# Kernel tuning notes

Hardware: AMD Instinct MI355X
Metric: run time of the kernel (lower is better)

Reference implementation:

```python
import jax, jax.numpy as jnp
import numpy as np

N = 50000      # nodes
F = 128        # feature_dim
H = 128        # hidden_dim
E = 1_600_000  # edges
G = 64         # graphs in batch
A = 8          # n_actions


def setup_inputs() -> dict:
    key = jax.random.key(0)
    ks = jax.random.split(key, 12)
    s = 0.05
    return {
        "x": jax.random.normal(ks[0], (N, F), jnp.float32),
        "edge_attr": jax.random.uniform(ks[1], (E, 1), jnp.float32),
        "W_e1": jax.random.normal(ks[2], (3, 1), jnp.float32) * s,
        "b_e1": jnp.zeros((1,), jnp.float32),
        "W_e2": jax.random.normal(ks[3], (1, 1), jnp.float32) * s,
        "b_e2": jnp.zeros((1,), jnp.float32),
        "W_gcn": jax.random.normal(ks[4], (F, H), jnp.float32) * s,
        "b_gcn": jnp.zeros((H,), jnp.float32),
        "W2": jax.random.normal(ks[5], (H, H), jnp.float32) * s,
        "b2": jnp.zeros((H,), jnp.float32),
        "W3": jax.random.normal(ks[6], (H, A), jnp.float32) * s,
        "b3": jnp.zeros((A,), jnp.float32),
        "edge_index": jax.random.randint(ks[7], (2, E), 0, N, jnp.int64),
        "batch": jnp.sort(jax.random.randint(ks[8], (N,), 0, G, jnp.int64)),
    }


def reference(x, edge_attr, W_e1, b_e1, W_e2, b_e2, W_gcn, b_gcn, W2, b2, W3, b3, edge_index, batch):
    # edge MLP: input is [src, dst, edge_attr] per edge -> (E, 3)
    e_feat = jnp.concatenate([edge_index.T.astype(x.dtype), edge_attr], axis=1)
    h = jax.nn.relu(e_feat @ W_e1 + b_e1)
    w = jax.nn.sigmoid(h @ W_e2 + b_e2)[:, 0]  # (E,)

    # GCNConv: add self-loops (weight 1), symmetric normalization
    loop = jnp.arange(N)
    row = jnp.concatenate([edge_index[0], loop])      # source
    col = jnp.concatenate([edge_index[1], loop])      # target
    w_all = jnp.concatenate([w, jnp.ones((N,), w.dtype)])
    deg = jax.ops.segment_sum(w_all, col, num_segments=N)
    safe_deg = jnp.where(deg > 0, deg, 1.0)
    dis = jnp.where(deg > 0, 1.0 / jnp.sqrt(safe_deg), 0.0)  # deg^-1/2, inf->0
    norm = dis[row] * w_all * dis[col]                # (E+N,)

    xw = x @ W_gcn                                    # (N, H)
    msg = norm[:, None] * xw[row]                     # (E+N, H) gather
    conv = jax.ops.segment_sum(msg, col, num_segments=N) + b_gcn  # scatter
    h1 = jax.nn.relu(conv)

    # global_mean_pool over batch index
    sums = jax.ops.segment_sum(h1, batch, num_segments=G)
    cnt = jax.ops.segment_sum(jnp.ones((N,), h1.dtype), batch, num_segments=G)
    pooled = sums / jnp.maximum(cnt, 1.0)[:, None]    # (G, H)

    h2 = jax.nn.relu(pooled @ W2 + b2)
    return h2 @ W3 + b3                               # (G, A)
```

## Files before the change

### kernel.cpp

```cpp
#include <hip/hip_runtime.h>
#include <hip/hip_fp16.h>
#include <math.h>

#define GB 64
#define AD 8
#define NC2 1024
#define BSH 6
#define BS  64
#define NBMAX 1024

typedef _Float16 half8 __attribute__((ext_vector_type(8)));
typedef float    f32x4 __attribute__((ext_vector_type(4)));

__global__ __launch_bounds__(256) void k_hist2(const int* __restrict__ ei,
                                               int* __restrict__ H2,
                                               int E, int ce, int NB) {
    __shared__ int h[NBMAX];
    int c = blockIdx.x;
    for (int b = threadIdx.x; b < NB; b += 256) h[b] = 0;
    __syncthreads();
    int e0 = c * ce, e1 = min(e0 + ce, E);
    int nv = (e1 - e0) & ~3;
    const int4* dst4 = (const int4*)(ei + E + e0);
    for (int v = threadIdx.x; v < (nv >> 2); v += 256) {
        int4 d = dst4[v];
        atomicAdd(&h[d.x >> BSH], 1);
        atomicAdd(&h[d.y >> BSH], 1);
        atomicAdd(&h[d.z >> BSH], 1);
        atomicAdd(&h[d.w >> BSH], 1);
    }
    for (int e = e0 + nv + threadIdx.x; e < e1; e += 256)
        atomicAdd(&h[ei[E + e] >> BSH], 1);
    __syncthreads();
    for (int b = threadIdx.x; b < NB; b += 256)
        H2[(size_t)c * NB + b] = h[b];
}

__global__ __launch_bounds__(256) void k_cscan(int* __restrict__ H2,
                                               int* __restrict__ cntB,
                                               int NB, int nc) {
    __shared__ int ssum[256];
    int b = blockIdx.x;
    int t = threadIdx.x;
    int v[4];
    int local = 0;
    #pragma unroll
    for (int k = 0; k < 4; k++) {
        int c = t * 4 + k;
        v[k] = (c < nc) ? H2[(size_t)c * NB + b] : 0;
        local += v[k];
    }
    ssum[t] = local;
    __syncthreads();
    for (int s = 1; s < 256; s <<= 1) {
        int tmp = (t >= s) ? ssum[t - s] : 0;
        __syncthreads();
        ssum[t] += tmp;
        __syncthreads();
    }
    int run = ssum[t] - local;
    #pragma unroll
    for (int k = 0; k < 4; k++) {
        int c = t * 4 + k;
        if (c < nc) H2[(size_t)c * NB + b] = run;
        run += v[k];
    }
    if (t == 255) cntB[b] = ssum[255];
}

__global__ __launch_bounds__(1024) void k_bscan(const int* __restrict__ cntB,
                                                int* __restrict__ bb,
                                                int* __restrict__ rowptr,
                                                float* __restrict__ psum,
                                                int NB, int n, int E) {
    __shared__ int sm[1024];
    int t = threadIdx.x;
    for (int z = t; z < GB * 128 + GB; z += 1024) psum[z] = 0.0f;
    int v = (t < NB) ? cntB[t] : 0;
    sm[t] = v;
    __syncthreads();
    for (int s = 1; s < 1024; s <<= 1) {
        int tmp = (t >= s) ? sm[t - s] : 0;
        __syncthreads();
        sm[t] += tmp;
        __syncthreads();
    }
    if (t < NB) bb[t] = sm[t] - v;
    if (t == NB - 1) bb[NB] = sm[t];
    if (t == 0) rowptr[n] = E;
}

__global__ __launch_bounds__(256) void k_fill2(const int* __restrict__ ei,
                                               const float* __restrict__ attr,
                                               const float* __restrict__ W_e1,
                                               const float* __restrict__ b_e1,
                                               const float* __restrict__ W_e2,
                                               const float* __restrict__ b_e2,
                                               const int* __restrict__ bb,
                                               const int* __restrict__ H2,
                                               int2* __restrict__ rec,
                                               int E, int ce, int NB) {
    __shared__ int off[NBMAX];
    int c = blockIdx.x;
    for (int b = threadIdx.x; b < NB; b += 256)
        off[b] = bb[b] + H2[(size_t)c * NB + b];
    __syncthreads();
    float w1s = W_e1[0], w1d = W_e1[1], w1a = W_e1[2], bb1 = b_e1[0];
    float w2 = W_e2[0], bb2 = b_e2[0];
    int e0 = c * ce, e1 = min(e0 + ce, E);
    int nv = (e1 - e0) & ~3;
    const int4*   src4 = (const int4*)(ei + e0);
    const int4*   dst4 = (const int4*)(ei + E + e0);
    const float4* att4 = (const float4*)(attr + e0);
    for (int v = threadIdx.x; v < (nv >> 2); v += 256) {
        int4 sv = src4[v];
        int4 dv = dst4[v];
        float4 av = att4[v];
        int   ss[4] = {sv.x, sv.y, sv.z, sv.w};
        int   dd[4] = {dv.x, dv.y, dv.z, dv.w};
        float aa[4] = {av.x, av.y, av.z, av.w};
        #pragma unroll
        for (int k = 0; k < 4; k++) {
            float h = fmaxf((float)ss[k] * w1s + (float)dd[k] * w1d + aa[k] * w1a + bb1, 0.0f);
            float w = 1.0f / (1.0f + expf(-(h * w2 + bb2)));
            int pos = atomicAdd(&off[dd[k] >> BSH], 1);
            int2 rv;
            rv.x = ss[k] | ((dd[k] & (BS - 1)) << 16);
            rv.y = __float_as_int(w);
            rec[pos] = rv;
        }
    }
    for (int e = e0 + nv + threadIdx.x; e < e1; e += 256) {
        int d = ei[E + e];
        int s = ei[e];
        float h = fmaxf((float)s * w1s + (float)d * w1d + attr[e] * w1a + bb1, 0.0f);
        float w = 1.0f / (1.0f + expf(-(h * w2 + bb2)));
        int pos = atomicAdd(&off[d >> BSH], 1);
        int2 rv;
        rv.x = s | ((d & (BS - 1)) << 16);
        rv.y = __float_as_int(w);
        rec[pos] = rv;
    }
}

__global__ __launch_bounds__(256) void k_bucket(const int2* __restrict__ rec,
                                                const int* __restrict__ bb,
                                                unsigned int* __restrict__ rec3,
                                                int* __restrict__ rowptr,
                                                float* __restrict__ dis, int n) {
    __shared__ int   cntL[BS];
    __shared__ float degL[BS];
    __shared__ int   pfx[BS];
    __shared__ int   cnt2[BS];
    int b = blockIdx.x;
    int t = threadIdx.x;
    if (t < BS) { cntL[t] = 0; degL[t] = 1.0f; cnt2[t] = 0; }
    __syncthreads();
    int s0 = bb[b], s1 = bb[b + 1];
    for (int j = s0 + t; j < s1; j += 256) {
        int2 rv = rec[j];
        int dl = (rv.x >> 16) & (BS - 1);
        atomicAdd(&cntL[dl], 1);
        atomicAdd(&degL[dl], __int_as_float(rv.y));
    }
    __syncthreads();
    if (t == 0) {
        int acc = 0;
        for (int k = 0; k < BS; k++) { pfx[k] = acc; acc += cntL[k]; }
    }
    __syncthreads();
    int lo = b << BSH;
    if (t < BS) {
        int i = lo + t;
        if (i < n) {
            rowptr[i] = s0 + pfx[t];
            dis[i] = rsqrtf(degL[t]);
        }
    }
    for (int j = s0 + t; j < s1; j += 256) {
        int2 rv = rec[j];
        int dl = (rv.x >> 16) & (BS - 1);
        int r = atomicAdd(&cnt2[dl], 1);
        unsigned int hh = (unsigned int)__half_as_ushort(
                              __float2half(__int_as_float(rv.y)));
        rec3[s0 + pfx[dl] + r] = (unsigned int)(rv.x & 0xFFFF) | (hh << 16);
    }
}

__global__ __launch_bounds__(256) void k_xw(const float* __restrict__ x,
                                            const float* __restrict__ Wg,
                                            const float* __restrict__ dis,
                                            __half* __restrict__ xwh, int n) {
    __shared__ _Float16 Wh[128 * 136];
    int tid = threadIdx.x;
    for (int idx = tid; idx < 128 * 128; idx += 256) {
        int k = idx >> 7, c = idx & 127;
        Wh[c * 136 + k] = (_Float16)Wg[idx];
    }
    __syncthreads();

    int lane = tid & 63;
    int w = tid >> 6;
    int n16 = lane & 15;
    int quad = lane >> 4;
    int r0 = blockIdx.x * 64 + w * 16;
    int arow = min(r0 + n16, n - 1);
    const float* xrow = x + (size_t)arow * 128;

    f32x4 acc[8];
    #pragma unroll
    for (int nt = 0; nt < 8; nt++) acc[nt] = (f32x4){0.f, 0.f, 0.f, 0.f};

    #pragma unroll
    for (int kk = 0; kk < 4; kk++) {
        int k0 = kk * 32 + quad * 8;
        float4 f0 = *(const float4*)(xrow + k0);
        float4 f1 = *(const float4*)(xrow + k0 + 4);
        half8 a;
        a[0] = (_Float16)f0.x; a[1] = (_Float16)f0.y;
        a[2] = (_Float16)f0.z; a[3] = (_Float16)f0.w;
        a[4] = (_Float16)f1.x; a[5] = (_Float16)f1.y;
        a[6] = (_Float16)f1.z; a[7] = (_Float16)f1.w;
        #pragma unroll
        for (int nt = 0; nt < 8; nt++) {
            half8 b = *(const half8*)&Wh[(nt * 16 + n16) * 136 + k0];
            acc[nt] = __builtin_amdgcn_mfma_f32_16x16x32_f16(a, b, acc[nt], 0, 0, 0);
        }
    }

    #pragma unroll
    for (int r = 0; r < 4; r++) {
        int row = r0 + quad * 4 + r;
        if (row < n) {
            float dv = dis[row];
            #pragma unroll
            for (int nt = 0; nt < 8; nt++)
                xwh[(size_t)row * 128 + nt * 16 + n16] = __float2half(acc[nt][r] * dv);
        }
    }
}

__global__ __launch_bounds__(256) void k_gather(const unsigned int* __restrict__ rec3,
                                                const int* __restrict__ rowptr,
                                                const float* __restrict__ dis,
                                                const __half* __restrict__ xh,
                                                const float* __restrict__ bg,
                                                __half* __restrict__ conv, int n) {
    int wave = threadIdx.x >> 6;
    int lane = threadIdx.x & 63;
    int g = lane >> 4;
    int q = lane & 15;
    int i = blockIdx.x * 4 + wave;
    if (i >= n) return;
    int st = rowptr[i];
    int m = rowptr[i + 1] - st;
    float di = dis[i];
    float acc[8];
    {
        uint4 sr = *(const uint4*)(xh + (size_t)i * 128 + q * 8);
        const __half2* hp = (const __half2*)&sr;
        float sc = (g == 0) ? 1.0f : 0.0f;
        #pragma unroll
        for (int k = 0; k < 4; k++) {
            float2 f = __half22float2(hp[k]);
            acc[2 * k]     = sc * f.x;
            acc[2 * k + 1] = sc * f.y;
        }
    }
    for (int base = 0; base < m; base += 64) {
        int kk = min(64, m - base);
        unsigned int rv = 0u;
        if (lane < kk) rv = rec3[st + base + lane];
        int jn = (kk + 3) >> 2;
        #pragma unroll 8
        for (int j = 0; j < jn; j++) {
            unsigned int rvj = (unsigned int)__builtin_amdgcn_ds_bpermute(
                                   ((j << 2) + g) << 2, (int)rv);
            int s = rvj & 0xFFFF;
            float cf = __half2float(__ushort_as_half((unsigned short)(rvj >> 16)));
            uint4 rw = *(const uint4*)(xh + (size_t)s * 128 + q * 8);
            const __half2* rp = (const __half2*)&rw;
            #pragma unroll
            for (int k = 0; k < 4; k++) {
                float2 f = __half22float2(rp[k]);
                acc[2 * k]     += cf * f.x;
                acc[2 * k + 1] += cf * f.y;
            }
        }
    }
    #pragma unroll
    for (int k = 0; k < 8; k++) {
        acc[k] += __shfl_xor(acc[k], 16);
        acc[k] += __shfl_xor(acc[k], 32);
    }
    if (g == 0) {
        float4 b0 = *(const float4*)(bg + q * 8);
        float4 b1 = *(const float4*)(bg + q * 8 + 4);
        const float* bp = (const float*)&b0;
        float v[8];
        #pragma unroll
        for (int k = 0; k < 4; k++) v[k] = fmaxf(di * acc[k] + bp[k], 0.0f);
        bp = (const float*)&b1;
        #pragma unroll
        for (int k = 0; k < 4; k++) v[4 + k] = fmaxf(di * acc[4 + k] + bp[k], 0.0f);
        __half2 h[4];
        #pragma unroll
        for (int k = 0; k < 4; k++)
            h[k] = __halves2half2(__float2half(v[2 * k]), __float2half(v[2 * k + 1]));
        uint4 o;
        o.x = *(unsigned int*)&h[0];
        o.y = *(unsigned int*)&h[1];
        o.z = *(unsigned int*)&h[2];
        o.w = *(unsigned int*)&h[3];
        *(uint4*)(conv + (size_t)i * 128 + q * 8) = o;
    }
}

__global__ __launch_bounds__(128) void k_pool(const __half* __restrict__ h1,
                                              const int* __restrict__ batch,
                                              float* __restrict__ psum,
                                              float* __restrict__ pcnt, int n) {
    int f = threadIdx.x;
    int n0 = blockIdx.x * 64;
    if (n0 >= n) return;
    int n1 = min(n0 + 64, n);
    int cur = batch[n0];
    float acc = 0.0f, cnt = 0.0f;
    for (int i = n0; i < n1; i++) {
        int g = batch[i];
        if (g != cur) {
            atomicAdd(&psum[cur * 128 + f], acc);
            if (f == 0) atomicAdd(&pcnt[cur], cnt);
            acc = 0.0f; cnt = 0.0f; cur = g;
        }
        acc += __half2float(h1[(size_t)i * 128 + f]);
        cnt += 1.0f;
    }
    atomicAdd(&psum[cur * 128 + f], acc);
    if (f == 0) atomicAdd(&pcnt[cur], cnt);
}

__global__ __launch_bounds__(128) void k_head(const float* __restrict__ psum,
                                              const float* __restrict__ pcnt,
                                              const float* __restrict__ W2,
                                              const float* __restrict__ b2,
                                              const float* __restrict__ W3,
                                              const float* __restrict__ b3,
                                              float* __restrict__ out) {
    __shared__ float pl[128];
    __shared__ float h2s[128];
    int g = blockIdx.x;
    int t = threadIdx.x;
    float c = fmaxf(pcnt[g], 1.0f);
    pl[t] = psum[g * 128 + t] / c;
    __syncthreads();
    float acc = b2[t];
    for (int k = 0; k < 128; k++) acc += pl[k] * W2[k * 128 + t];
    h2s[t] = fmaxf(acc, 0.0f);
    __syncthreads();
    if (t < AD) {
        float o = b3[t];
        for (int k = 0; k < 128; k++) o += h2s[k] * W3[k * AD + t];
        out[g * AD + t] = o;
    }
}

extern "C" void kernel_launch(void* const* d_in, const int* in_sizes, int n_in,
                              void* d_out, int out_size, void* d_ws, size_t ws_size,
                              hipStream_t stream) {
    const float* x        = (const float*)d_in[0];
    const float* edge_attr= (const float*)d_in[1];
    const float* W_e1     = (const float*)d_in[2];
    const float* b_e1     = (const float*)d_in[3];
    const float* W_e2     = (const float*)d_in[4];
    const float* b_e2     = (const float*)d_in[5];
    const float* W_gcn    = (const float*)d_in[6];
    const float* b_gcn    = (const float*)d_in[7];
    const float* W2       = (const float*)d_in[8];
    const float* b2       = (const float*)d_in[9];
    const float* W3       = (const float*)d_in[10];
    const float* b3       = (const float*)d_in[11];
    const int*   ei       = (const int*)d_in[12];
    const int*   batch    = (const int*)d_in[13];
    float* out = (float*)d_out;

    const int E  = in_sizes[12] / 2;
    const int n  = in_sizes[13];
    const int NB = (n + BS - 1) >> BSH;
    const int ce = (((E + NC2 - 1) / NC2) + 3) & ~3;

    char* p = (char*)d_ws;
    __half* xwh   = (__half*)p;  p += (size_t)n * 128 * sizeof(__half);
    int*    H2    = (int*)p;
    __half* conv  = (__half*)p;  p += (size_t)n * 128 * sizeof(__half);
    int2*   rec   = (int2*)p;    p += (size_t)E * sizeof(int2);
    unsigned int* rec3 = (unsigned int*)p; p += (size_t)E * sizeof(unsigned int);
    float*  dis   = (float*)p;   p += (size_t)n * sizeof(float);
    float*  psum  = (float*)p;   p += (size_t)GB * 128 * sizeof(float);
    float*  pcnt  = (float*)p;   p += (size_t)GB * sizeof(float);
    int*    rowptr= (int*)p;     p += (size_t)(n + 1) * sizeof(int);
    int*    cntB  = (int*)p;     p += (size_t)NBMAX * sizeof(int);
    int*    bb    = (int*)p;     p += (size_t)(NBMAX + 1) * sizeof(int);

    k_hist2<<<NC2, 256, 0, stream>>>(ei, H2, E, ce, NB);
    k_cscan<<<NB, 256, 0, stream>>>(H2, cntB, NB, NC2);
    k_bscan<<<1, 1024, 0, stream>>>(cntB, bb, rowptr, psum, NB, n, E);
    k_fill2<<<NC2, 256, 0, stream>>>(ei, edge_attr, W_e1, b_e1, W_e2, b_e2,
                                     bb, H2, rec, E, ce, NB);
    k_bucket<<<NB, 256, 0, stream>>>(rec, bb, rec3, rowptr, dis, n);
    k_xw<<<(n + 63) / 64, 256, 0, stream>>>(x, W_gcn, dis, xwh, n);
    k_gather<<<(n + 3) / 4, 256, 0, stream>>>(rec3, rowptr, dis, xwh,
                                              b_gcn, conv, n);
    k_pool<<<(n + 63) / 64, 128, 0, stream>>>(conv, batch, psum, pcnt, n);
    k_head<<<GB, 128, 0, stream>>>(psum, pcnt, W2, b2, W3, b3, out);
}
```

Before: 253.1 us.

## Coarsen edge chunks, amortize weight staging in xw, regroup pooling per graph

The edge counting-sort chunk count drops from 1024 to 256, with 512-thread blocks for the histogram and fill kernels. This shrinks the per-chunk histogram matrix and the column scan, which now takes one value per thread. k_xw handles 128 rows per block, so the shared fp16 weight tile is built once for twice the rows. Global mean pooling now uses a grid of graphs × 4 chunks: binary search on the sorted batch finds each graph's segment, and a block reduction leaves only one atomic per feature per block. The cost is fewer, larger blocks in the histogram, fill and xw kernels, which may lower occupancy, and longer per-block work in the fill phase.

```diff
diff --git a/kernel.cpp b/kernel.cpp
--- a/kernel.cpp
+++ b/kernel.cpp
@@ -4,7 +4,7 @@
 
 #define GB 64
 #define AD 8
-#define NC2 1024
+#define NC2 256
 #define BSH 6
 #define BS  64
 #define NBMAX 1024
@@ -12,27 +12,27 @@
 typedef _Float16 half8 __attribute__((ext_vector_type(8)));
 typedef float    f32x4 __attribute__((ext_vector_type(4)));
 
-__global__ __launch_bounds__(256) void k_hist2(const int* __restrict__ ei,
+__global__ __launch_bounds__(512) void k_hist2(const int* __restrict__ ei,
                                                int* __restrict__ H2,
                                                int E, int ce, int NB) {
     __shared__ int h[NBMAX];
     int c = blockIdx.x;
-    for (int b = threadIdx.x; b < NB; b += 256) h[b] = 0;
+    for (int b = threadIdx.x; b < NB; b += 512) h[b] = 0;
     __syncthreads();
     int e0 = c * ce, e1 = min(e0 + ce, E);
     int nv = (e1 - e0) & ~3;
     const int4* dst4 = (const int4*)(ei + E + e0);
-    for (int v = threadIdx.x; v < (nv >> 2); v += 256) {
+    for (int v = threadIdx.x; v < (nv >> 2); v += 512) {
         int4 d = dst4[v];
         atomicAdd(&h[d.x >> BSH], 1);
         atomicAdd(&h[d.y >> BSH], 1);
         atomicAdd(&h[d.z >> BSH], 1);
         atomicAdd(&h[d.w >> BSH], 1);
     }
-    for (int e = e0 + nv + threadIdx.x; e < e1; e += 256)
+    for (int e = e0 + nv + threadIdx.x; e < e1; e += 512)
         atomicAdd(&h[ei[E + e] >> BSH], 1);
     __syncthreads();
-    for (int b = threadIdx.x; b < NB; b += 256)
+    for (int b = threadIdx.x; b < NB; b += 512)
         H2[(size_t)c * NB + b] = h[b];
 }
 
@@ -42,15 +42,8 @@
     __shared__ int ssum[256];
     int b = blockIdx.x;
     int t = threadIdx.x;
-    int v[4];
-    int local = 0;
-    #pragma unroll
-    for (int k = 0; k < 4; k++) {
-        int c = t * 4 + k;
-        v[k] = (c < nc) ? H2[(size_t)c * NB + b] : 0;
-        local += v[k];
-    }
-    ssum[t] = local;
+    int v = (t < nc) ? H2[(size_t)t * NB + b] : 0;
+    ssum[t] = v;
     __syncthreads();
     for (int s = 1; s < 256; s <<= 1) {
         int tmp = (t >= s) ? ssum[t - s] : 0;
@@ -58,13 +51,7 @@
         ssum[t] += tmp;
         __syncthreads();
     }
-    int run = ssum[t] - local;
-    #pragma unroll
-    for (int k = 0; k < 4; k++) {
-        int c = t * 4 + k;
-        if (c < nc) H2[(size_t)c * NB + b] = run;
-        run += v[k];
-    }
+    if (t < nc) H2[(size_t)t * NB + b] = ssum[t] - v;
     if (t == 255) cntB[b] = ssum[255];
 }
 
@@ -90,7 +77,7 @@
     if (t == 0) rowptr[n] = E;
 }
 
-__global__ __launch_bounds__(256) void k_fill2(const int* __restrict__ ei,
+__global__ __launch_bounds__(512) void k_fill2(const int* __restrict__ ei,
                                                const float* __restrict__ attr,
                                                const float* __restrict__ W_e1,
                                                const float* __restrict__ b_e1,
@@ -102,7 +89,7 @@
                                                int E, int ce, int NB) {
     __shared__ int off[NBMAX];
     int c = blockIdx.x;
-    for (int b = threadIdx.x; b < NB; b += 256)
+    for (int b = threadIdx.x; b < NB; b += 512)
         off[b] = bb[b] + H2[(size_t)c * NB + b];
     __syncthreads();
     float w1s = W_e1[0], w1d = W_e1[1], w1a = W_e1[2], bb1 = b_e1[0];
@@ -112,7 +99,7 @@
     const int4*   src4 = (const int4*)(ei + e0);
     const int4*   dst4 = (const int4*)(ei + E + e0);
     const float4* att4 = (const float4*)(attr + e0);
-    for (int v = threadIdx.x; v < (nv >> 2); v += 256) {
+    for (int v = threadIdx.x; v < (nv >> 2); v += 512) {
         int4 sv = src4[v];
         int4 dv = dst4[v];
         float4 av = att4[v];
@@ -130,7 +117,7 @@
             rec[pos] = rv;
         }
     }
-    for (int e = e0 + nv + threadIdx.x; e < e1; e += 256) {
+    for (int e = e0 + nv + threadIdx.x; e < e1; e += 512) {
         int d = ei[E + e];
         int s = ei[e];
         float h = fmaxf((float)s * w1s + (float)d * w1d + attr[e] * w1a + bb1, 0.0f);
@@ -203,39 +190,44 @@
     int w = tid >> 6;
     int n16 = lane & 15;
     int quad = lane >> 4;
-    int r0 = blockIdx.x * 64 + w * 16;
-    int arow = min(r0 + n16, n - 1);
-    const float* xrow = x + (size_t)arow * 128;
-
-    f32x4 acc[8];
+
     #pragma unroll
-    for (int nt = 0; nt < 8; nt++) acc[nt] = (f32x4){0.f, 0.f, 0.f, 0.f};
-
-    #pragma unroll
-    for (int kk = 0; kk < 4; kk++) {
-        int k0 = kk * 32 + quad * 8;
-        float4 f0 = *(const float4*)(xrow + k0);
-        float4 f1 = *(const float4*)(xrow + k0 + 4);
-        half8 a;
-        a[0] = (_Float16)f0.x; a[1] = (_Float16)f0.y;
-        a[2] = (_Float16)f0.z; a[3] = (_Float16)f0.w;
-        a[4] = (_Float16)f1.x; a[5] = (_Float16)f1.y;
-        a[6] = (_Float16)f1.z; a[7] = (_Float16)f1.w;
-        #pragma unroll
-        for (int nt = 0; nt < 8; nt++) {
-            half8 b = *(const half8*)&Wh[(nt * 16 + n16) * 136 + k0];
-            acc[nt] = __builtin_amdgcn_mfma_f32_16x16x32_f16(a, b, acc[nt], 0, 0, 0);
-        }
-    }
-
-    #pragma unroll
-    for (int r = 0; r < 4; r++) {
-        int row = r0 + quad * 4 + r;
-        if (row < n) {
-            float dv = dis[row];
+    for (int hf = 0; hf < 2; hf++) {
+        int r0 = blockIdx.x * 128 + hf * 64 + w * 16;
+        if (r0 >= n) break;
+        int arow = min(r0 + n16, n - 1);
+        const float* xrow = x + (size_t)arow * 128;
+
+        f32x4 acc[8];
+        #pragma unroll
+        for (int nt = 0; nt < 8; nt++) acc[nt] = (f32x4){0.f, 0.f, 0.f, 0.f};
+
+        #pragma unroll
+        for (int kk = 0; kk < 4; kk++) {
+            int k0 = kk * 32 + quad * 8;
+            float4 f0 = *(const float4*)(xrow + k0);
+            float4 f1 = *(const float4*)(xrow + k0 + 4);
+            half8 a;
+            a[0] = (_Float16)f0.x; a[1] = (_Float16)f0.y;
+            a[2] = (_Float16)f0.z; a[3] = (_Float16)f0.w;
+            a[4] = (_Float16)f1.x; a[5] = (_Float16)f1.y;
+            a[6] = (_Float16)f1.z; a[7] = (_Float16)f1.w;
             #pragma unroll
-            for (int nt = 0; nt < 8; nt++)
-                xwh[(size_t)row * 128 + nt * 16 + n16] = __float2half(acc[nt][r] * dv);
+            for (int nt = 0; nt < 8; nt++) {
+                half8 b = *(const half8*)&Wh[(nt * 16 + n16) * 136 + k0];
+                acc[nt] = __builtin_amdgcn_mfma_f32_16x16x32_f16(a, b, acc[nt], 0, 0, 0);
+            }
+        }
+
+        #pragma unroll
+        for (int r = 0; r < 4; r++) {
+            int row = r0 + quad * 4 + r;
+            if (row < n) {
+                float dv = dis[row];
+                #pragma unroll
+                for (int nt = 0; nt < 8; nt++)
+                    xwh[(size_t)row * 128 + nt * 16 + n16] = __float2half(acc[nt][r] * dv);
+            }
         }
     }
 }
@@ -316,28 +308,39 @@
     }
 }
 
-__global__ __launch_bounds__(128) void k_pool(const __half* __restrict__ h1,
+__device__ __forceinline__ int lbound(const int* __restrict__ a, int n, int v) {
+    int lo = 0, hi = n;
+    while (lo < hi) {
+        int mid = (lo + hi) >> 1;
+        if (a[mid] < v) lo = mid + 1; else hi = mid;
+    }
+    return lo;
+}
+
+__global__ __launch_bounds__(256) void k_pool(const __half* __restrict__ h1,
                                               const int* __restrict__ batch,
                                               float* __restrict__ psum,
                                               float* __restrict__ pcnt, int n) {
-    int f = threadIdx.x;
-    int n0 = blockIdx.x * 64;
-    if (n0 >= n) return;
-    int n1 = min(n0 + 64, n);
-    int cur = batch[n0];
-    float acc = 0.0f, cnt = 0.0f;
-    for (int i = n0; i < n1; i++) {
-        int g = batch[i];
-        if (g != cur) {
-            atomicAdd(&psum[cur * 128 + f], acc);
-            if (f == 0) atomicAdd(&pcnt[cur], cnt);
-            acc = 0.0f; cnt = 0.0f; cur = g;
-        }
-        acc += __half2float(h1[(size_t)i * 128 + f]);
-        cnt += 1.0f;
-    }
-    atomicAdd(&psum[cur * 128 + f], acc);
-    if (f == 0) atomicAdd(&pcnt[cur], cnt);
+    int g = blockIdx.x, ch = blockIdx.y;
+    int t = threadIdx.x;
+    int s = lbound(batch, n, g);
+    int e = lbound(batch, n, g + 1);
+    int rq = t >> 6, q = t & 63;
+    float ax = 0.0f, ay = 0.0f;
+    for (int i = s + ch * 4 + rq; i < e; i += 16) {
+        __half2 hv = *(const __half2*)(h1 + (size_t)i * 128 + 2 * q);
+        float2 f = __half22float2(hv);
+        ax += f.x; ay += f.y;
+    }
+    __shared__ float2 sm[256];
+    sm[t] = make_float2(ax, ay);
+    __syncthreads();
+    if (t < 64) {
+        float2 a0 = sm[t], a1 = sm[t + 64], a2 = sm[t + 128], a3 = sm[t + 192];
+        atomicAdd(&psum[g * 128 + 2 * q],     a0.x + a1.x + a2.x + a3.x);
+        atomicAdd(&psum[g * 128 + 2 * q + 1], a0.y + a1.y + a2.y + a3.y);
+    }
+    if (ch == 0 && t == 0) pcnt[g] = (float)(e - s);
 }
 
 __global__ __launch_bounds__(128) void k_head(const float* __restrict__ psum,
@@ -402,15 +405,15 @@
     int*    cntB  = (int*)p;     p += (size_t)NBMAX * sizeof(int);
     int*    bb    = (int*)p;     p += (size_t)(NBMAX + 1) * sizeof(int);
 
-    k_hist2<<<NC2, 256, 0, stream>>>(ei, H2, E, ce, NB);
+    k_hist2<<<NC2, 512, 0, stream>>>(ei, H2, E, ce, NB);
     k_cscan<<<NB, 256, 0, stream>>>(H2, cntB, NB, NC2);
     k_bscan<<<1, 1024, 0, stream>>>(cntB, bb, rowptr, psum, NB, n, E);
-    k_fill2<<<NC2, 256, 0, stream>>>(ei, edge_attr, W_e1, b_e1, W_e2, b_e2,
+    k_fill2<<<NC2, 512, 0, stream>>>(ei, edge_attr, W_e1, b_e1, W_e2, b_e2,
                                      bb, H2, rec, E, ce, NB);
     k_bucket<<<NB, 256, 0, stream>>>(rec, bb, rec3, rowptr, dis, n);
-    k_xw<<<(n + 63) / 64, 256, 0, stream>>>(x, W_gcn, dis, xwh, n);
+    k_xw<<<(n + 127) / 128, 256, 0, stream>>>(x, W_gcn, dis, xwh, n);
     k_gather<<<(n + 3) / 4, 256, 0, stream>>>(rec3, rowptr, dis, xwh,
                                               b_gcn, conv, n);
-    k_pool<<<(n + 63) / 64, 128, 0, stream>>>(conv, batch, psum, pcnt, n);
+    k_pool<<<dim3(GB, 4), 256, 0, stream>>>(conv, batch, psum, pcnt, n);
     k_head<<<GB, 128, 0, stream>>>(psum, pcnt, W2, b2, W3, b3, out);
 }
```

Measured after the change: 235.3 us. -7.0%, faster.
